# Performance work log

Hardware: AMD Instinct MI355X
Metric: run time of the kernel (lower is better)

The kernel has to match this reference:

```python
import jax, jax.numpy as jnp
import numpy as np

HEAD_SIZE = 64  # n_embds // n_heads = 1024 // 16

def setup_inputs() -> dict:
    key = jax.random.key(0)
    k0, k1, k2, k3 = jax.random.split(key, 4)
    B, S, D, H = 4, 4096, 1024, HEAD_SIZE
    scale = 1.0 / np.sqrt(D)
    return {
        "decoder_input": jax.random.normal(k0, (B, S, D), dtype=jnp.float32),
        "Wq": jax.random.normal(k1, (D, H), dtype=jnp.float32) * scale,
        "Wk": jax.random.normal(k2, (D, H), dtype=jnp.float32) * scale,
        "Wv": jax.random.normal(k3, (D, H), dtype=jnp.float32) * scale,
    }

def reference(decoder_input, Wq, Wk, Wv):
    # q,k,v: [B,S,H]; Linear(bias=False) == x @ W
    q = decoder_input @ Wq
    k = decoder_input @ Wk
    v = decoder_input @ Wv
    head_size = k.shape[2]
    # scores: [B,S,S] -- full materialization, as in the original
    scores = jnp.einsum('bqh,bkh->bqk', q, k) / jnp.sqrt(jnp.float32(head_size))
    S = scores.shape[1]
    causal = jnp.tril(jnp.ones((S, S), dtype=bool))  # lower-triangular mask
    masked = jnp.where(causal, scores, -jnp.inf)
    attn = jax.nn.softmax(masked, axis=2)
    # dropout_rate = 0.0 -> identity
    return jnp.einsum('bqk,bkh->bqh', attn, v)
```

## Files before the change

kernel.cpp:

```cpp
#include <hip/hip_runtime.h>
#include <hip/hip_bf16.h>
#include <math.h>

typedef __bf16 bf16_t;
typedef __bf16 bf16x8 __attribute__((ext_vector_type(8)));
typedef float f32x4 __attribute__((ext_vector_type(4)));

constexpr int SS = 4096;
constexpr int DD = 1024;
constexpr int HH = 64;

#if __has_builtin(__builtin_amdgcn_exp2f)
#define EXP2F __builtin_amdgcn_exp2f
#else
#define EXP2F exp2f
#endif

static __device__ __forceinline__ f32x4 mfma16(bf16x8 a, bf16x8 b, f32x4 c) {
  return __builtin_amdgcn_mfma_f32_16x16x32_bf16(a, b, c, 0, 0, 0);
}

__global__ __launch_bounds__(256) void prep_w(const float* __restrict__ wq,
                                              const float* __restrict__ wk,
                                              const float* __restrict__ wv,
                                              bf16_t* __restrict__ wt) {
  __shared__ float ls[64 * 68];
  int tid = threadIdx.x;
  int sel = blockIdx.x >> 4, kb = blockIdx.x & 15, k0 = kb * 64;
  const float* src = (sel == 0) ? wq : ((sel == 1) ? wk : wv);
  int bn = sel * 64;
#pragma unroll
  for (int i = 0; i < 4; ++i) {
    int e = tid + i * 256;
    int r = e >> 4, c4 = (e & 15) * 4;
    *(float4*)&ls[r * 68 + c4] = *(const float4*)(src + (size_t)(k0 + r) * 64 + c4);
  }
  __syncthreads();
#pragma unroll
  for (int j = 0; j < 2; ++j) {
    int e = tid + j * 256;
    int n = e >> 3, kg = e & 7;
    bf16x8 v;
#pragma unroll
    for (int t = 0; t < 8; ++t) v[t] = (bf16_t)ls[(kg * 8 + t) * 68 + n];
    *(bf16x8*)(wt + (size_t)(bn + n) * 1024 + k0 + kg * 8) = v;
  }
}

__global__ __launch_bounds__(256) void gemm_qkv(const float* __restrict__ x,
                                                const bf16_t* __restrict__ wt,
                                                bf16_t* __restrict__ qo,
                                                bf16_t* __restrict__ ko,
                                                bf16_t* __restrict__ vto) {
  __shared__ bf16_t xs[2][64 * 64];
  __shared__ bf16_t wsh[2][96 * 64];
  int tid = threadIdx.x;
  int wave = tid >> 6, lane = tid & 63, quad = lane >> 4, ml = lane & 15;
  int mblk = blockIdx.x >> 1, nhalf = blockIdx.x & 1;
  int m0 = mblk * 64;
  int nbase = nhalf * 96;

  f32x4 acc[6];
#pragma unroll
  for (int i = 0; i < 6; ++i) acc[i] = (f32x4){0.f, 0.f, 0.f, 0.f};

  int xrow = tid >> 2, xseg = tid & 3;
  float4 xr[4];
  bf16x8 wr[3];

  auto load_g = [&](int k0) {
    const float* p = x + (size_t)(m0 + xrow) * DD + k0 + xseg * 16;
    xr[0] = *(const float4*)p;
    xr[1] = *(const float4*)(p + 4);
    xr[2] = *(const float4*)(p + 8);
    xr[3] = *(const float4*)(p + 12);
#pragma unroll
    for (int i = 0; i < 3; ++i) {
      int c = tid + i * 256;
      int r = c >> 3, cc = c & 7;
      wr[i] = *(const bf16x8*)(wt + (size_t)(nbase + r) * DD + k0 + cc * 8);
    }
  };
  auto store_lds = [&](int bf) {
    bf16x8 v0, v1;
    v0[0] = (bf16_t)xr[0].x; v0[1] = (bf16_t)xr[0].y;
    v0[2] = (bf16_t)xr[0].z; v0[3] = (bf16_t)xr[0].w;
    v0[4] = (bf16_t)xr[1].x; v0[5] = (bf16_t)xr[1].y;
    v0[6] = (bf16_t)xr[1].z; v0[7] = (bf16_t)xr[1].w;
    v1[0] = (bf16_t)xr[2].x; v1[1] = (bf16_t)xr[2].y;
    v1[2] = (bf16_t)xr[2].z; v1[3] = (bf16_t)xr[2].w;
    v1[4] = (bf16_t)xr[3].x; v1[5] = (bf16_t)xr[3].y;
    v1[6] = (bf16_t)xr[3].z; v1[7] = (bf16_t)xr[3].w;
    int cc0 = (2 * xseg) ^ (xrow & 7);
    int cc1 = (2 * xseg + 1) ^ (xrow & 7);
    *(bf16x8*)&xs[bf][xrow * 64 + cc0 * 8] = v0;
    *(bf16x8*)&xs[bf][xrow * 64 + cc1 * 8] = v1;
#pragma unroll
    for (int i = 0; i < 3; ++i) {
      int c = tid + i * 256;
      int r = c >> 3, cc = c & 7;
      *(bf16x8*)&wsh[bf][r * 64 + ((cc ^ (r & 7)) * 8)] = wr[i];
    }
  };

  load_g(0);
  store_lds(0);
  load_g(64);
  __syncthreads();
  for (int it = 0; it < 16; ++it) {
    int bf = it & 1;
#pragma unroll
    for (int s = 0; s < 2; ++s) {
      int rchunk = ((s * 4 + quad) ^ (ml & 7)) * 8;
      bf16x8 a = *(const bf16x8*)&xs[bf][(wave * 16 + ml) * 64 + rchunk];
#pragma unroll
      for (int i = 0; i < 6; ++i) {
        bf16x8 bfr = *(const bf16x8*)&wsh[bf][(i * 16 + ml) * 64 + rchunk];
        acc[i] = mfma16(a, bfr, acc[i]);
      }
    }
    if (it < 15) {
      store_lds(1 - bf);
      if (it < 14) load_g((it + 2) * 64);
      __syncthreads();
    }
  }

  int b = m0 >> 12;
  int sr = m0 & 4095;
  const float QSCALE = 0.18033688011112042f;
  bf16_t* vls = (bf16_t*)wsh;
#pragma unroll
  for (int i = 0; i < 6; ++i) {
    int col = nbase + i * 16 + ml;
#pragma unroll
    for (int r = 0; r < 4; ++r) {
      int lrow = wave * 16 + quad * 4 + r;
      size_t grow = (size_t)b * SS + sr + lrow;
      if (col < 64) qo[grow * HH + col] = (bf16_t)(acc[i][r] * QSCALE);
      else if (col < 128) ko[grow * HH + (col - 64)] = (bf16_t)(acc[i][r]);
      else vls[(col - 128) * 72 + lrow] = (bf16_t)(acc[i][r]);
    }
  }
  __syncthreads();
  if (nhalf == 1) {
    int h = tid >> 2, sg = tid & 3;
    *(bf16x8*)(vto + ((size_t)b * HH + h) * SS + sr + sg * 16) =
        *(const bf16x8*)&vls[h * 72 + sg * 16];
    *(bf16x8*)(vto + ((size_t)b * HH + h) * SS + sr + sg * 16 + 8) =
        *(const bf16x8*)&vls[h * 72 + sg * 16 + 8];
  }
}

__global__ __launch_bounds__(256) void attn_partial(const bf16_t* __restrict__ qg,
                                                    const bf16_t* __restrict__ kg,
                                                    const bf16_t* __restrict__ vg,
                                                    float* __restrict__ partO,
                                                    float* __restrict__ lb,
                                                    float* __restrict__ out) {
  __shared__ bf16_t Kl[2][64 * 64];
  __shared__ bf16_t Vl[2][64 * 64];
  __shared__ bf16_t Pl[4][16 * 64];
  int tid = threadIdx.x;
  int wave = tid >> 6, lane = tid & 63, quad = lane >> 4, ml = lane & 15;

  int bid = blockIdx.x;
  int b, jt, c0, len, slot = 0;
  bool direct;
  if (bid < 768) {
    jt = 63 - (bid >> 4);
    int rem = bid & 15;
    b = rem >> 2;
    int ch = rem & 3;
    int L = (jt + 4) >> 2;
    c0 = ch * L;
    int c1 = c0 + L; if (c1 > jt + 1) c1 = jt + 1;
    len = c1 - c0;
    slot = (b * 48 + (jt - 16)) * 4 + ch;
    direct = false;
  } else {
    int idx = bid - 768;
    jt = 15 - (idx >> 2);
    b = idx & 3;
    c0 = 0;
    len = jt + 1;
    direct = true;
  }
  int q0 = jt * 64;

  const bf16_t* qb = qg + (size_t)b * SS * HH;
  const bf16_t* kb = kg + (size_t)b * SS * HH;
  const bf16_t* vb = vg + (size_t)b * HH * SS;

  int qrow = q0 + wave * 16 + ml;
  bf16x8 aq0 = *(const bf16x8*)(qb + (size_t)qrow * HH + quad * 8);
  bf16x8 aq1 = *(const bf16x8*)(qb + (size_t)qrow * HH + 32 + quad * 8);

  bf16x8 kreg[2], vreg[2];
  int srl = tid >> 3, scc = tid & 7;
  auto load_kv = [&](int kt) {
#pragma unroll
    for (int i = 0; i < 2; ++i) {
      int r = srl + i * 32;
      kreg[i] = *(const bf16x8*)(kb + (size_t)(kt * 64 + r) * HH + scc * 8);
      vreg[i] = *(const bf16x8*)(vb + (size_t)r * SS + kt * 64 + scc * 8);
    }
  };
  auto store_kv = [&](int bf) {
#pragma unroll
    for (int i = 0; i < 2; ++i) {
      int r = srl + i * 32;
      int off = r * 64 + ((scc ^ (r & 7)) * 8);
      *(bf16x8*)&Kl[bf][off] = kreg[i];
      *(bf16x8*)&Vl[bf][off] = vreg[i];
    }
  };

  f32x4 oa[4];
#pragma unroll
  for (int i = 0; i < 4; ++i) oa[i] = (f32x4){0.f, 0.f, 0.f, 0.f};
  float lr[4] = {0.f, 0.f, 0.f, 0.f};

  load_kv(c0);
  store_kv(0);

  for (int i = 0; i < len; ++i) {
    int kt = c0 + i;
    int bf = i & 1;
    __syncthreads();
    if (i + 1 < len) load_kv(kt + 1);

    f32x4 sa[4];
#pragma unroll
    for (int nt = 0; nt < 4; ++nt) sa[nt] = (f32x4){0.f, 0.f, 0.f, 0.f};
#pragma unroll
    for (int s = 0; s < 2; ++s) {
      bf16x8 a = s ? aq1 : aq0;
      int rchunk = ((s * 4 + quad) ^ (ml & 7)) * 8;
#pragma unroll
      for (int nt = 0; nt < 4; ++nt) {
        bf16x8 bfr = *(const bf16x8*)&Kl[bf][(nt * 16 + ml) * 64 + rchunk];
        sa[nt] = mfma16(a, bfr, sa[nt]);
      }
    }

    if (kt == jt) {
#pragma unroll
      for (int nt = 0; nt < 4; ++nt) {
        int key = kt * 64 + nt * 16 + ml;
#pragma unroll
        for (int r = 0; r < 4; ++r) {
          int qr = q0 + wave * 16 + quad * 4 + r;
          if (key > qr) sa[nt][r] = -3.38953139e38f;
        }
      }
    }

#pragma unroll
    for (int r = 0; r < 4; ++r) {
      float p0 = EXP2F(sa[0][r]);
      float p1 = EXP2F(sa[1][r]);
      float p2 = EXP2F(sa[2][r]);
      float p3 = EXP2F(sa[3][r]);
      sa[0][r] = p0; sa[1][r] = p1; sa[2][r] = p2; sa[3][r] = p3;
      lr[r] += (p0 + p1) + (p2 + p3);
    }

#pragma unroll
    for (int nt = 0; nt < 4; ++nt) {
#pragma unroll
      for (int r = 0; r < 4; ++r) {
        int row = quad * 4 + r;
        int cc = nt * 2 + (ml >> 3);
        Pl[wave][row * 64 + ((cc ^ (row & 7)) * 8) + (ml & 7)] = (bf16_t)sa[nt][r];
      }
    }
#pragma unroll
    for (int s = 0; s < 2; ++s) {
      int rchunk = ((s * 4 + quad) ^ (ml & 7)) * 8;
      bf16x8 pa = *(const bf16x8*)&Pl[wave][ml * 64 + rchunk];
#pragma unroll
      for (int ht = 0; ht < 4; ++ht) {
        bf16x8 bv = *(const bf16x8*)&Vl[bf][(ht * 16 + ml) * 64 + rchunk];
        oa[ht] = mfma16(pa, bv, oa[ht]);
      }
    }

    if (i + 1 < len) store_kv(1 - bf);
  }

#pragma unroll
  for (int r = 0; r < 4; ++r) {
    float t = lr[r];
    t += __shfl_xor(t, 1);
    t += __shfl_xor(t, 2);
    t += __shfl_xor(t, 4);
    t += __shfl_xor(t, 8);
    lr[r] = t;
  }

  if (direct) {
#pragma unroll
    for (int r = 0; r < 4; ++r) {
      float inv = 1.0f / lr[r];
      int row = q0 + wave * 16 + quad * 4 + r;
#pragma unroll
      for (int ht = 0; ht < 4; ++ht)
        out[((size_t)b * SS + row) * HH + ht * 16 + ml] = oa[ht][r] * inv;
    }
  } else {
    float* po = partO + (size_t)slot * 4096;
#pragma unroll
    for (int r = 0; r < 4; ++r) {
      int row = wave * 16 + quad * 4 + r;
#pragma unroll
      for (int ht = 0; ht < 4; ++ht)
        po[row * 64 + ht * 16 + ml] = oa[ht][r];
      if (ml == 0) lb[slot * 64 + row] = lr[r];
    }
  }
}

__global__ __launch_bounds__(256) void combine(const float* __restrict__ partO,
                                               const float* __restrict__ lb,
                                               float* __restrict__ out) {
  int bid = blockIdx.x;
  int b = bid / 96;
  int rest = bid - b * 96;
  int jt = 16 + (rest >> 1), half = rest & 1;
  int base = (b * 48 + (jt - 16)) * 4;
  int tid = threadIdx.x;
  int lr_ = tid >> 3, cb = tid & 7;
  int row = half * 32 + lr_;

  float l = 0.f;
  float4 o0 = {0.f, 0.f, 0.f, 0.f}, o1 = {0.f, 0.f, 0.f, 0.f};
#pragma unroll
  for (int c = 0; c < 4; ++c) {
    l += lb[(base + c) * 64 + row];
    const float* p = partO + (size_t)(base + c) * 4096 + row * 64 + cb * 8;
    float4 a = *(const float4*)p;
    float4 bq = *(const float4*)(p + 4);
    o0.x += a.x; o0.y += a.y; o0.z += a.z; o0.w += a.w;
    o1.x += bq.x; o1.y += bq.y; o1.z += bq.z; o1.w += bq.w;
  }
  float inv = 1.0f / l;
  float* op = out + (((size_t)b * SS) + jt * 64 + row) * HH + cb * 8;
  o0.x *= inv; o0.y *= inv; o0.z *= inv; o0.w *= inv;
  o1.x *= inv; o1.y *= inv; o1.z *= inv; o1.w *= inv;
  *(float4*)op = o0;
  *(float4*)(op + 4) = o1;
}

extern "C" void kernel_launch(void* const* d_in, const int* in_sizes, int n_in,
                              void* d_out, int out_size, void* d_ws, size_t ws_size,
                              hipStream_t stream) {
  const float* x  = (const float*)d_in[0];
  const float* wq = (const float*)d_in[1];
  const float* wk = (const float*)d_in[2];
  const float* wv = (const float*)d_in[3];
  float* out = (float*)d_out;

  char* wsb = (char*)d_ws;
  bf16_t* wt  = (bf16_t*)wsb;
  bf16_t* q   = (bf16_t*)(wsb + 524288);
  bf16_t* k   = (bf16_t*)(wsb + 2621440);
  bf16_t* vt  = (bf16_t*)(wsb + 4718592);
  float*  po  = (float*)(wsb + 6815744);
  float*  lb  = (float*)(wsb + 19398656);

  prep_w<<<48, 256, 0, stream>>>(wq, wk, wv, wt);
  gemm_qkv<<<512, 256, 0, stream>>>(x, wt, q, k, vt);
  attn_partial<<<832, 256, 0, stream>>>(q, k, vt, po, lb, out);
  combine<<<384, 256, 0, stream>>>(po, lb, out);
}
```

Measured before the change: 151.4 us.

## Use variable split-KV chunking per query tile and single-buffer K/V LDS

Replaces the fixed 4-way split over key tiles (for query tiles 16+) with a graded split of 1, 2, 4 or 8 chunks that grows with the query tile index. This raises the block count from 832 to 1376 and evens out per-block work across the causal triangle. K/V shared memory goes from double- to single-buffered, with an extra barrier per iteration, to cut LDS use and raise occupancy. The combine kernel now handles a variable chunk count, at the cost of more partial-output traffic and less overlap between loads and compute.

```diff
diff --git a/kernel.cpp b/kernel.cpp
--- a/kernel.cpp
+++ b/kernel.cpp
@@ -158,34 +158,26 @@
                                                     float* __restrict__ partO,
                                                     float* __restrict__ lb,
                                                     float* __restrict__ out) {
-  __shared__ bf16_t Kl[2][64 * 64];
-  __shared__ bf16_t Vl[2][64 * 64];
+  __shared__ bf16_t Kl[64 * 64];
+  __shared__ bf16_t Vl[64 * 64];
   __shared__ bf16_t Pl[4][16 * 64];
   int tid = threadIdx.x;
   int wave = tid >> 6, lane = tid & 63, quad = lane >> 4, ml = lane & 15;
 
   int bid = blockIdx.x;
-  int b, jt, c0, len, slot = 0;
-  bool direct;
-  if (bid < 768) {
-    jt = 63 - (bid >> 4);
-    int rem = bid & 15;
-    b = rem >> 2;
-    int ch = rem & 3;
-    int L = (jt + 4) >> 2;
-    c0 = ch * L;
-    int c1 = c0 + L; if (c1 > jt + 1) c1 = jt + 1;
-    len = c1 - c0;
-    slot = (b * 48 + (jt - 16)) * 4 + ch;
-    direct = false;
-  } else {
-    int idx = bid - 768;
-    jt = 15 - (idx >> 2);
-    b = idx & 3;
-    c0 = 0;
-    len = jt + 1;
-    direct = true;
-  }
+  int b = bid & 3;
+  int j = 343 - (bid >> 2);
+  int jt, ch, nch;
+  if (j < 8)        { jt = j;                   ch = 0;            nch = 1; }
+  else if (j < 24)  { jt = 8  + ((j - 8) >> 1); ch = (j - 8) & 1;  nch = 2; }
+  else if (j < 88)  { jt = 16 + ((j - 24) >> 2); ch = (j - 24) & 3; nch = 4; }
+  else              { jt = 32 + ((j - 88) >> 3); ch = (j - 88) & 7; nch = 8; }
+  int L = (jt + nch) / nch;
+  int c0 = ch * L;
+  int c1 = c0 + L; if (c1 > jt + 1) c1 = jt + 1;
+  int len = c1 - c0;
+  bool direct = (nch == 1);
+  int slot = b * 336 + (j - 8);
   int q0 = jt * 64;
 
   const bf16_t* qb = qg + (size_t)b * SS * HH;
@@ -206,13 +198,13 @@
       vreg[i] = *(const bf16x8*)(vb + (size_t)r * SS + kt * 64 + scc * 8);
     }
   };
-  auto store_kv = [&](int bf) {
+  auto store_kv = [&]() {
 #pragma unroll
     for (int i = 0; i < 2; ++i) {
       int r = srl + i * 32;
       int off = r * 64 + ((scc ^ (r & 7)) * 8);
-      *(bf16x8*)&Kl[bf][off] = kreg[i];
-      *(bf16x8*)&Vl[bf][off] = vreg[i];
+      *(bf16x8*)&Kl[off] = kreg[i];
+      *(bf16x8*)&Vl[off] = vreg[i];
     }
   };
 
@@ -222,11 +214,11 @@
   float lr[4] = {0.f, 0.f, 0.f, 0.f};
 
   load_kv(c0);
-  store_kv(0);
 
   for (int i = 0; i < len; ++i) {
     int kt = c0 + i;
-    int bf = i & 1;
+    __syncthreads();
+    store_kv();
     __syncthreads();
     if (i + 1 < len) load_kv(kt + 1);
 
@@ -239,7 +231,7 @@
       int rchunk = ((s * 4 + quad) ^ (ml & 7)) * 8;
 #pragma unroll
       for (int nt = 0; nt < 4; ++nt) {
-        bf16x8 bfr = *(const bf16x8*)&Kl[bf][(nt * 16 + ml) * 64 + rchunk];
+        bf16x8 bfr = *(const bf16x8*)&Kl[(nt * 16 + ml) * 64 + rchunk];
         sa[nt] = mfma16(a, bfr, sa[nt]);
       }
     }
@@ -281,12 +273,10 @@
       bf16x8 pa = *(const bf16x8*)&Pl[wave][ml * 64 + rchunk];
 #pragma unroll
       for (int ht = 0; ht < 4; ++ht) {
-        bf16x8 bv = *(const bf16x8*)&Vl[bf][(ht * 16 + ml) * 64 + rchunk];
+        bf16x8 bv = *(const bf16x8*)&Vl[(ht * 16 + ml) * 64 + rchunk];
         oa[ht] = mfma16(pa, bv, oa[ht]);
       }
     }
-
-    if (i + 1 < len) store_kv(1 - bf);
   }
 
 #pragma unroll
@@ -325,31 +315,30 @@
                                                const float* __restrict__ lb,
                                                float* __restrict__ out) {
   int bid = blockIdx.x;
-  int b = bid / 96;
-  int rest = bid - b * 96;
-  int jt = 16 + (rest >> 1), half = rest & 1;
-  int base = (b * 48 + (jt - 16)) * 4;
+  int b = bid / 56;
+  int jt = 8 + (bid - b * 56);
+  int nch, jbase;
+  if (jt < 16)      { nch = 2; jbase = 8 + 2 * (jt - 8); }
+  else if (jt < 32) { nch = 4; jbase = 24 + 4 * (jt - 16); }
+  else              { nch = 8; jbase = 88 + 8 * (jt - 32); }
+  int base = b * 336 + (jbase - 8);
   int tid = threadIdx.x;
-  int lr_ = tid >> 3, cb = tid & 7;
-  int row = half * 32 + lr_;
+  int row = tid >> 2, cb = tid & 3;
 
   float l = 0.f;
-  float4 o0 = {0.f, 0.f, 0.f, 0.f}, o1 = {0.f, 0.f, 0.f, 0.f};
-#pragma unroll
-  for (int c = 0; c < 4; ++c) {
+  f32x4 o[4];
+#pragma unroll
+  for (int jj = 0; jj < 4; ++jj) o[jj] = (f32x4){0.f, 0.f, 0.f, 0.f};
+  for (int c = 0; c < nch; ++c) {
     l += lb[(base + c) * 64 + row];
-    const float* p = partO + (size_t)(base + c) * 4096 + row * 64 + cb * 8;
-    float4 a = *(const float4*)p;
-    float4 bq = *(const float4*)(p + 4);
-    o0.x += a.x; o0.y += a.y; o0.z += a.z; o0.w += a.w;
-    o1.x += bq.x; o1.y += bq.y; o1.z += bq.z; o1.w += bq.w;
+    const f32x4* p = (const f32x4*)(partO + (size_t)(base + c) * 4096 + row * 64 + cb * 16);
+#pragma unroll
+    for (int jj = 0; jj < 4; ++jj) o[jj] += p[jj];
   }
   float inv = 1.0f / l;
-  float* op = out + (((size_t)b * SS) + jt * 64 + row) * HH + cb * 8;
-  o0.x *= inv; o0.y *= inv; o0.z *= inv; o0.w *= inv;
-  o1.x *= inv; o1.y *= inv; o1.z *= inv; o1.w *= inv;
-  *(float4*)op = o0;
-  *(float4*)(op + 4) = o1;
+  f32x4* op = (f32x4*)(out + (((size_t)b * SS) + jt * 64 + row) * HH + cb * 16);
+#pragma unroll
+  for (int jj = 0; jj < 4; ++jj) op[jj] = o[jj] * inv;
 }
 
 extern "C" void kernel_launch(void* const* d_in, const int* in_sizes, int n_in,
@@ -367,10 +356,10 @@
   bf16_t* k   = (bf16_t*)(wsb + 2621440);
   bf16_t* vt  = (bf16_t*)(wsb + 4718592);
   float*  po  = (float*)(wsb + 6815744);
-  float*  lb  = (float*)(wsb + 19398656);
+  float*  lb  = (float*)(wsb + 28835840);
 
   prep_w<<<48, 256, 0, stream>>>(wq, wk, wv, wt);
   gemm_qkv<<<512, 256, 0, stream>>>(x, wt, q, k, vt);
-  attn_partial<<<832, 256, 0, stream>>>(q, k, vt, po, lb, out);
-  combine<<<384, 256, 0, stream>>>(po, lb, out);
-}
+  attn_partial<<<1376, 256, 0, stream>>>(q, k, vt, po, lb, out);
+  combine<<<224, 256, 0, stream>>>(po, lb, out);
+}
```

Result: faster. 147.8 us (-2.4%).
